# Optimization experiments

Measured on AMD Instinct MI355X. Metric: run time of the kernel, lower is better.

The kernel has to match this reference:

```python
import jax, jax.numpy as jnp
import numpy as np

H_SZ, W_SZ = 24, 24  # size for location=2 (H*W == N3)

def _ln(x, g, b, eps=1e-5):
    m = jnp.mean(x, axis=-1, keepdims=True)
    v = jnp.var(x, axis=-1, keepdims=True)
    return (x - m) / jnp.sqrt(v + eps) * g + b

def _cross_attn(value, x2, Wp, bp):
    # key = softmax(x2^T, dim=1) == softmax over channels; query = softmax over tokens
    k = jax.nn.softmax(x2, axis=2)   # [B,M,C], softmax over C
    q = jax.nn.softmax(x2, axis=1)   # [B,M,C], softmax over M
    ctx = jnp.einsum('bnc,bmc->bnm', value, k)   # value @ key
    att = jnp.einsum('bnm,bmc->bnc', ctx, q)     # context @ query
    return att @ Wp.T + bp

def _dwconv(x, Wdw, bdw, Hh, Ww):
    B, N, C = x.shape
    t = x.transpose(0, 2, 1).reshape(B, C, Hh, Ww)
    y = jax.lax.conv_general_dilated(t, Wdw, (1, 1), 'SAME',
                                     feature_group_count=C,
                                     dimension_numbers=('NCHW', 'OIHW', 'NCHW'))
    y = y + bdw[None, :, None, None]
    return y.reshape(B, C, N).transpose(0, 2, 1)

def setup_inputs() -> dict:
    key = jax.random.key(0)
    ks = jax.random.split(key, 16)
    B = 4; d0, d1, d2 = 128, 256, 512
    N1, N2, N3 = 96 * 96, 48 * 48, 24 * 24
    s = 0.02
    dh = 4 * d2
    inp = {}
    inp['x']  = jax.random.normal(ks[0], (B, N1, d0), jnp.float32)
    inp['x2'] = jax.random.normal(ks[1], (B, N2, d1), jnp.float32)
    inp['x3'] = jax.random.normal(ks[2], (B, N3, d2), jnp.float32)
    inp['W_lin']  = jax.random.normal(ks[3], (d2, d0)) * s   # linear: d0->d2
    inp['W_lin2'] = jax.random.normal(ks[4], (d2, d1)) * s   # linear2: d1->d2
    inp['W_lin3'] = jax.random.normal(ks[5], (d1, d0)) * s   # linear3: d0->d1
    inp['W_lin4'] = jax.random.normal(ks[6], (d2, d1)) * s   # linear4: d1->d2
    inp['w'] = jnp.ones((1,), jnp.float32)
    inp['Wp1'] = jax.random.normal(ks[7], (d2, d2)) * s;  inp['bp1'] = jnp.zeros((d2,))
    inp['Wp2'] = jax.random.normal(ks[8], (d2, d2)) * s;  inp['bp2'] = jnp.zeros((d2,))
    inp['Wp3'] = jax.random.normal(ks[9], (d1, d1)) * s;  inp['bp3'] = jnp.zeros((d1,))
    inp['Wp4'] = jax.random.normal(ks[10], (d2, d2)) * s; inp['bp4'] = jnp.zeros((d2,))
    inp['g_norm'] = jnp.ones((d2,)); inp['b_norm'] = jnp.zeros((d2,))
    inp['Wfc1'] = jax.random.normal(ks[11], (dh, d2)) * s; inp['bfc1'] = jnp.zeros((dh,))
    inp['Wdw']  = jax.random.normal(ks[12], (dh, 1, 3, 3)) * s; inp['bdw'] = jnp.zeros((dh,))
    inp['g_ln1'] = jnp.ones((dh,)); inp['b_ln1'] = jnp.zeros((dh,))
    inp['Wfc2'] = jax.random.normal(ks[13], (d2, dh)) * s; inp['bfc2'] = jnp.zeros((d2,))
    return inp

def reference(x, x2, x3, W_lin, W_lin2, W_lin3, W_lin4, w,
              Wp1, bp1, Wp2, bp2, Wp3, bp3, Wp4, bp4,
              g_norm, b_norm, Wfc1, bfc1, Wdw, bdw, g_ln1, b_ln1, Wfc2, bfc2):
    # location == 2 branch
    image  = x  @ W_lin.T    # [B,N1,d2]
    image2 = x2 @ W_lin2.T   # [B,N2,d2]
    image4 = x  @ W_lin3.T   # [B,N1,d1]
    atten1 = _cross_attn(x3, image,  Wp1, bp1)
    atten2 = _cross_attn(x3, image2, Wp2, bp2)
    a3 = _cross_attn(x2, image4, Wp3, bp3)   # [B,N2,d1]
    a3 = a3 @ W_lin4.T                        # [B,N2,d2]
    atten3 = _cross_attn(x3, a3, Wp4, bp4)    # [B,N3,d2]
    f = jax.nn.sigmoid(w)
    other = (1.0 - f) / 2.0
    atten_ = f * atten3 + other * atten2 + other * atten1
    atten = x3 + atten_
    an = _ln(atten, g_norm, b_norm)
    # MixFFN_skip (fc1 computed once; torch computes it twice with same result)
    h = an @ Wfc1.T + bfc1
    dw = _dwconv(h, Wdw, bdw, H_SZ, W_SZ)
    ax = jax.nn.gelu(_ln(dw + h, g_ln1, b_ln1), approximate=False)
    out = ax @ Wfc2.T + bfc2
    return atten + out
```

## Files before the change

### kernel.cpp

```cpp
#include <hip/hip_runtime.h>
#include <hip/hip_bf16.h>
#include <math.h>

typedef long long i64;
typedef __attribute__((ext_vector_type(8))) short short8v;
typedef __attribute__((ext_vector_type(4))) float float4v;

#define SPITCH 72
#define NCV 13

__device__ __forceinline__ float ldv(const void* p, i64 idx, int isBf16) {
  return isBf16 ? __bfloat162float(((const __hip_bfloat16*)p)[idx])
                : ((const float*)p)[idx];
}
__device__ __forceinline__ unsigned short bf16bits(float f) {
  __hip_bfloat16 h = __float2bfloat16(f);
  return *(unsigned short*)&h;
}
__device__ __forceinline__ float bits2f(unsigned short u) {
  union { unsigned int ui; float fl; } cv; cv.ui = ((unsigned int)u) << 16;
  return cv.fl;
}

__global__ void detect_dtype(const unsigned short* w, int* dt) {
  dt[0] = (w[0] == 0) ? 0 : 1;
}

struct CvArgs {
  const void* src[NCV];
  unsigned short* dst[NCV];
  i64 n[NCV];
  int blkStart[NCV + 1];
};
__global__ __launch_bounds__(256) void convert_many(const int* dt, CvArgs a) {
  int au = dt[0];
  int bid = blockIdx.x;
  int lo = 0;
  #pragma unroll
  for (int i = 0; i < NCV; ++i) if (bid >= a.blkStart[i + 1]) lo = i + 1;
  const void* s = a.src[lo];
  unsigned short* d = a.dst[lo];
  i64 n = a.n[lo];
  i64 base = ((i64)(bid - a.blkStart[lo]) * 256 + threadIdx.x) * 4;
  if (base + 4 <= n) {
    #pragma unroll
    for (int j = 0; j < 4; ++j) d[base + j] = bf16bits(ldv(s, base + j, au));
  } else {
    for (; base < n; ++base) d[base] = bf16bits(ldv(s, base, au));
  }
}

__global__ void transpose_dw(const int* dt, const void* Wdw, unsigned short* Wdwt) {
  int au = dt[0];
  int i = blockIdx.x * 256 + threadIdx.x;
  if (i >= 9 * 2048) return;
  int k = i / 2048, ch = i % 2048;
  Wdwt[i] = bf16bits(ldv(Wdw, (i64)ch * 9 + k, au));
}

__global__ __launch_bounds__(256) void gemm_mfma_bt(
    const int* dt,
    const unsigned short* A, i64 bsA,
    const unsigned short* Bt, i64 bsB,
    const void* bias, int biasDt,
    const void* add, int addDt, i64 bsAdd,
    void* C, i64 bsC, int outMode,
    int M, int N, int K, int flags,
    const void* wPtr, int alphaMode,
    float* csP, float* rsP)
{
  __shared__ unsigned short Ash[64 * SPITCH];
  __shared__ unsigned short Bsh[64 * SPITCH];
  __shared__ unsigned short LT[64 * SPITCH];

  const int au = dt[0];
  const int bDt = (biasDt == 2) ? au : biasDt;
  const int aDt = (addDt == 2) ? au : addDt;

  const int b  = blockIdx.z;
  const int m0 = blockIdx.y * 64;
  const int n0 = blockIdx.x * 64;
  const int t = threadIdx.x;
  const int lane = t & 63, wave = t >> 6;
  const int wr = (wave >> 1) * 32, wc = (wave & 1) * 32;
  const int quad = lane >> 4, l15 = lane & 15;
  const unsigned short* Ab = A + (i64)b * bsA;
  const unsigned short* Bb = Bt + (i64)b * bsB;
  const int sr = t >> 3, sg = (t & 7) * 8;

  float alpha = 1.0f;
  if (alphaMode) {
    float w0 = ldv(wPtr, 0, au);
    float f = 1.0f / (1.0f + expf(-w0));
    alpha = (alphaMode == 2) ? f : (1.0f - f) * 0.5f;
  }

  float4v acc00 = {0.f,0.f,0.f,0.f}, acc01 = {0.f,0.f,0.f,0.f};
  float4v acc10 = {0.f,0.f,0.f,0.f}, acc11 = {0.f,0.f,0.f,0.f};

  for (int k0 = 0; k0 < K; k0 += 64) {
    #pragma unroll
    for (int p = 0; p < 2; ++p) {
      int rr = sr + p * 32;
      *(short8v*)&Ash[rr * SPITCH + sg] = *(const short8v*)&Ab[(i64)(m0 + rr) * K + k0 + sg];
      *(short8v*)&Bsh[rr * SPITCH + sg] = *(const short8v*)&Bb[(i64)(n0 + rr) * K + k0 + sg];
    }
    __syncthreads();
    #pragma unroll
    for (int ks = 0; ks < 2; ++ks) {
      int ko = ks * 32 + quad * 8;
      short8v a0 = *(const short8v*)&Ash[(wr + l15) * SPITCH + ko];
      short8v a1 = *(const short8v*)&Ash[(wr + 16 + l15) * SPITCH + ko];
      short8v b0 = *(const short8v*)&Bsh[(wc + l15) * SPITCH + ko];
      short8v b1 = *(const short8v*)&Bsh[(wc + 16 + l15) * SPITCH + ko];
      acc00 = __builtin_amdgcn_mfma_f32_16x16x32_bf16(a0, b0, acc00, 0, 0, 0);
      acc01 = __builtin_amdgcn_mfma_f32_16x16x32_bf16(a0, b1, acc01, 0, 0, 0);
      acc10 = __builtin_amdgcn_mfma_f32_16x16x32_bf16(a1, b0, acc10, 0, 0, 0);
      acc11 = __builtin_amdgcn_mfma_f32_16x16x32_bf16(a1, b1, acc11, 0, 0, 0);
    }
    __syncthreads();
  }

  float* Cf = (float*)C;
  unsigned short* Ch = (unsigned short*)C;

  if (outMode == 2) {
    #pragma unroll
    for (int rg = 0; rg < 4; ++rg) {
      #pragma unroll
      for (int sub = 0; sub < 4; ++sub) {
        int lr = wr + quad * 4 + rg + (sub >> 1) * 16;
        int lc = wc + l15 + (sub & 1) * 16;
        float v = (sub == 0 ? acc00[rg] : sub == 1 ? acc01[rg] :
                   sub == 2 ? acc10[rg] : acc11[rg]) * alpha;
        if (bias) v += ldv(bias, n0 + lc, bDt);
        if (flags & 1) v = expf(v);
        LT[lc * SPITCH + lr] = bf16bits(v);
      }
    }
    __syncthreads();
    #pragma unroll
    for (int p = 0; p < 2; ++p) {
      int rr = sr + p * 32;
      short8v vv = *(short8v*)&LT[rr * SPITCH + sg];
      *(short8v*)(Ch + (i64)b * bsC + (i64)(n0 + rr) * M + m0 + sg) = vv;
    }
    if (csP) {
      if (t < 64) {
        const unsigned short* Lr = &LT[t * SPITCH];
        float s = 0.f;
        #pragma unroll
        for (int i = 0; i < 64; ++i) s += bits2f(Lr[i]);
        atomicAdd(&csP[(i64)b * N + n0 + t], s);
      } else if (t < 128) {
        int tok = t - 64;
        float s = 0.f;
        #pragma unroll
        for (int i = 0; i < 64; ++i) s += bits2f(LT[i * SPITCH + tok]);
        atomicAdd(&rsP[(i64)b * M + m0 + tok], s);
      }
    }
    return;
  }

  #pragma unroll
  for (int rg = 0; rg < 4; ++rg) {
    #pragma unroll
    for (int sub = 0; sub < 4; ++sub) {
      int lr = wr + quad * 4 + rg + (sub >> 1) * 16;
      int lc = wc + l15 + (sub & 1) * 16;
      int gi = m0 + lr, gj = n0 + lc;
      float v = (sub == 0 ? acc00[rg] : sub == 1 ? acc01[rg] :
                 sub == 2 ? acc10[rg] : acc11[rg]) * alpha;
      if (bias) v += ldv(bias, gj, bDt);
      if (add)  v += ldv(add, (i64)b * bsAdd + (i64)gi * N + gj, aDt);
      i64 idx = (i64)b * bsC + (i64)gi * N + gj;
      if (flags & 2) v += Cf[idx];
      if (flags & 1) v = expf(v);
      if (outMode == 1) Ch[idx] = bf16bits(v);
      else              Cf[idx] = v;
    }
  }
}

__global__ __launch_bounds__(256, 2) void softprod128_db(
    const unsigned short* Gt, const float* rs, float* Sraw,
    int C, i64 M, int splits, int mChunk)
{
  __shared__ unsigned short Ash[2][128 * SPITCH];
  __shared__ unsigned short Bsh[2][128 * SPITCH];
  const int b  = blockIdx.z / splits;
  const int sp = blockIdx.z % splits;
  const int nStrips = C >> 7;
  int rem = blockIdx.x, s0 = 0;
  while (rem >= nStrips - s0) { rem -= nStrips - s0; ++s0; }
  const int s1 = s0 + rem;
  const int c0 = s0 * 128;
  const int c1 = s1 * 128;

  const int t = threadIdx.x;
  const int lane = t & 63, wave = t >> 6;
  const int wrow = (wave >> 1) * 64, wcol = (wave & 1) * 64;
  const int quad = lane >> 4, l15 = lane & 15;
  const unsigned short* Gb = Gt + (i64)b * C * M;
  const float* rib = rs + (i64)b * M;
  const int sg = (t & 7) * 8;
  const int r4 = t >> 3;

  float4v acc[4][4];
  #pragma unroll
  for (int i = 0; i < 4; ++i)
    #pragma unroll
    for (int j = 0; j < 4; ++j)
      acc[i][j] = (float4v){0.f, 0.f, 0.f, 0.f};

  const i64 mBeg = (i64)sp * mChunk;
  const int nt = mChunk >> 6;

  const unsigned short* Arow = &Gb[(i64)(c0 + r4) * M + sg];
  const unsigned short* Brow = &Gb[(i64)(c1 + r4) * M + sg];

  short8v pa[4], pb[4];
  float rv[8];
  {
    i64 m0 = mBeg;
    #pragma unroll
    for (int p = 0; p < 4; ++p) {
      pa[p] = *(const short8v*)&Arow[(i64)32 * p * M + m0];
      pb[p] = *(const short8v*)&Brow[(i64)32 * p * M + m0];
    }
    #pragma unroll
    for (int j = 0; j < 8; ++j) {
      float rr_ = rsqrtf(rib[m0 + sg + j]);
      rv[j] = rr_ * rr_;
    }
  }

  int cur = 0;
  for (int tt = 0; tt < nt; ++tt) {
    #pragma unroll
    for (int p = 0; p < 4; ++p) {
      *(short8v*)&Ash[cur][(r4 + 32 * p) * SPITCH + sg] = pa[p];
      short8v sb;
      #pragma unroll
      for (int j = 0; j < 8; ++j)
        sb[j] = (short)bf16bits(bits2f((unsigned short)pb[p][j]) * rv[j]);
      *(short8v*)&Bsh[cur][(r4 + 32 * p) * SPITCH + sg] = sb;
    }
    __syncthreads();
    if (tt + 1 < nt) {
      i64 m0 = mBeg + (i64)(tt + 1) * 64;
      #pragma unroll
      for (int p = 0; p < 4; ++p) {
        pa[p] = *(const short8v*)&Arow[(i64)32 * p * M + m0];
        pb[p] = *(const short8v*)&Brow[(i64)32 * p * M + m0];
      }
      #pragma unroll
      for (int j = 0; j < 8; ++j) {
        float rr_ = rsqrtf(rib[m0 + sg + j]);
        rv[j] = rr_ * rr_;
      }
    }
    #pragma unroll
    for (int ks = 0; ks < 2; ++ks) {
      int ko = ks * 32 + quad * 8;
      short8v af[4], bfr[4];
      #pragma unroll
      for (int i = 0; i < 4; ++i) {
        af[i]  = *(const short8v*)&Ash[cur][(wrow + i * 16 + l15) * SPITCH + ko];
        bfr[i] = *(const short8v*)&Bsh[cur][(wcol + i * 16 + l15) * SPITCH + ko];
      }
      #pragma unroll
      for (int i = 0; i < 4; ++i)
        #pragma unroll
        for (int j = 0; j < 4; ++j)
          acc[i][j] = __builtin_amdgcn_mfma_f32_16x16x32_bf16(af[i], bfr[j], acc[i][j], 0, 0, 0);
    }
    cur ^= 1;
  }

  float* Sb = Sraw + (i64)b * C * C;
  #pragma unroll
  for (int i = 0; i < 4; ++i)
    #pragma unroll
    for (int rg = 0; rg < 4; ++rg) {
      int r = c0 + wrow + i * 16 + quad * 4 + rg;
      #pragma unroll
      for (int j = 0; j < 4; ++j) {
        int cc = c1 + wcol + j * 16 + l15;
        atomicAdd(&Sb[(i64)r * C + cc], acc[i][j][rg]);
      }
    }
}

__global__ void scale_S_sym_bf16(const float* Sraw, const float* cs,
                                 unsigned short* Sb, int C, i64 total) {
  i64 i = (i64)blockIdx.x * blockDim.x + threadIdx.x;
  if (i >= total) return;
  i64 cc2 = (i64)C * C;
  i64 b = i / cc2;
  i64 r = (i % cc2) / C;
  int cp = (int)(i % C);
  const float* Sb_ = Sraw + b * cc2;
  float v = (((int)r >> 6) <= (cp >> 6)) ? Sb_[r * C + cp] : Sb_[(i64)cp * C + r];
  Sb[i] = bf16bits(v / cs[b * C + cp]);
}

__global__ __launch_bounds__(256) void transpose_to_bf16(
    const float* T, unsigned short* Tt, int Nn) {
  __shared__ float tile[64][65];
  int b = blockIdx.z;
  int i0 = blockIdx.y * 64, j0 = blockIdx.x * 64;
  const float* Tb = T + (i64)b * Nn * Nn;
  unsigned short* Ttb = Tt + (i64)b * Nn * Nn;
  int t = threadIdx.x;
  int li = t >> 6, lj = t & 63;
  #pragma unroll
  for (int p = 0; p < 16; ++p)
    tile[li + p * 4][lj] = Tb[(i64)(i0 + li + p * 4) * Nn + j0 + lj];
  __syncthreads();
  #pragma unroll
  for (int p = 0; p < 16; ++p) {
    int row = li + p * 4;
    Ttb[(i64)(j0 + row) * Nn + i0 + lj] = bf16bits(tile[lj][row]);
  }
}

__global__ void combine_bias(const int* dt, const void* w, const void* bp1,
                             const void* bp2, const void* bp4, float* biasc) {
  int au = dt[0];
  int j = threadIdx.x;
  float w0 = ldv(w, 0, au);
  float f = 1.0f / (1.0f + expf(-w0));
  float other = (1.0f - f) * 0.5f;
  biasc[j] = f * ldv(bp4, j, au) + other * (ldv(bp1, j, au) + ldv(bp2, j, au));
}

__global__ __launch_bounds__(256) void layernorm512(const int* dt, const float* X,
                                                    const void* g, const void* be,
                                                    __hip_bfloat16* Y) {
  int au = dt[0];
  i64 row = blockIdx.x;
  const float* xr = X + row * 512;
  int t = threadIdx.x;
  float x0 = xr[t], x1 = xr[t + 256];
  float s = x0 + x1, q = x0 * x0 + x1 * x1;
  #pragma unroll
  for (int off = 32; off; off >>= 1) { s += __shfl_down(s, off); q += __shfl_down(q, off); }
  __shared__ float ws_[4], wq_[4];
  int lane = t & 63, wv = t >> 6;
  if (!lane) { ws_[wv] = s; wq_[wv] = q; }
  __syncthreads();
  float S = ws_[0] + ws_[1] + ws_[2] + ws_[3];
  float Q = wq_[0] + wq_[1] + wq_[2] + wq_[3];
  float mean = S * (1.f / 512.f);
  float var = Q * (1.f / 512.f) - mean * mean;
  float inv = rsqrtf(var + 1e-5f);
  Y[row * 512 + t]       = __float2bfloat16((x0 - mean) * inv * ldv(g, t, au) + ldv(be, t, au));
  Y[row * 512 + t + 256] = __float2bfloat16((x1 - mean) * inv * ldv(g, t + 256, au) + ldv(be, t + 256, au));
}

__global__ __launch_bounds__(256) void dwconv_ln_gelu(
    const int* dt,
    const unsigned short* h, const unsigned short* Wdwt, const void* bdw,
    const void* g, const void* be, unsigned short* ax)
{
  int au = dt[0];
  int n = blockIdx.x;
  int b = blockIdx.y;
  int y = n / 24, x = n % 24;
  const unsigned short* hb = h + (i64)b * 576 * 2048;
  int t = threadIdx.x;
  int ch0 = t * 8;

  float accv[8];
  #pragma unroll
  for (int j = 0; j < 8; ++j) accv[j] = ldv(bdw, ch0 + j, au);

  #pragma unroll
  for (int dy = 0; dy < 3; ++dy) {
    int yy = y + dy - 1;
    if (yy < 0 || yy >= 24) continue;
    #pragma unroll
    for (int dx = 0; dx < 3; ++dx) {
      int xx = x + dx - 1;
      if (xx < 0 || xx >= 24) continue;
      short8v hv = *(const short8v*)&hb[(i64)(yy * 24 + xx) * 2048 + ch0];
      short8v wv = *(const short8v*)&Wdwt[(i64)(dy * 3 + dx) * 2048 + ch0];
      #pragma unroll
      for (int j = 0; j < 8; ++j)
        accv[j] += bits2f((unsigned short)hv[j]) * bits2f((unsigned short)wv[j]);
    }
  }

  short8v hc = *(const short8v*)&hb[(i64)n * 2048 + ch0];
  float z[8];
  float s = 0.f, q = 0.f;
  #pragma unroll
  for (int j = 0; j < 8; ++j) {
    float zz = accv[j] + bits2f((unsigned short)hc[j]);
    z[j] = zz; s += zz; q += zz * zz;
  }

  #pragma unroll
  for (int off = 32; off; off >>= 1) { s += __shfl_down(s, off); q += __shfl_down(q, off); }
  __shared__ float ws_[4], wq_[4];
  int lane = t & 63, wv2 = t >> 6;
  if (!lane) { ws_[wv2] = s; wq_[wv2] = q; }
  __syncthreads();
  float S = ws_[0] + ws_[1] + ws_[2] + ws_[3];
  float Q = wq_[0] + wq_[1] + wq_[2] + wq_[3];
  float mean = S * (1.f / 2048.f);
  float var = Q * (1.f / 2048.f) - mean * mean;
  float inv = rsqrtf(var + 1e-5f);

  short8v ov;
  #pragma unroll
  for (int j = 0; j < 8; ++j) {
    float v = (z[j] - mean) * inv * ldv(g, ch0 + j, au) + ldv(be, ch0 + j, au);
    float gl = 0.5f * v * (1.0f + erff(v * 0.70710678118654752f));
    ov[j] = (short)bf16bits(gl);
  }
  *(short8v*)&ax[((i64)b * 576 + n) * 2048 + ch0] = ov;
}

extern "C" void kernel_launch(void* const* d_in, const int* in_sizes, int n_in,
                              void* d_out, int out_size, void* d_ws, size_t ws_size,
                              hipStream_t stream) {
  const int B = 4, N1 = 9216, N2 = 2304, N3 = 576;
  const int d0 = 128, d1 = 256, d2 = 512, dh = 2048;

  const void* x     = d_in[0];
  const void* x2    = d_in[1];
  const void* x3    = d_in[2];
  const void* Wlin  = d_in[3];
  const void* Wlin2 = d_in[4];
  const void* Wlin3 = d_in[5];
  const void* Wlin4 = d_in[6];
  const void* w     = d_in[7];
  const void* Wp1 = d_in[8];  const void* bp1 = d_in[9];
  const void* Wp2 = d_in[10]; const void* bp2 = d_in[11];
  const void* Wp3 = d_in[12]; const void* bp3 = d_in[13];
  const void* Wp4 = d_in[14]; const void* bp4 = d_in[15];
  const void* gnorm = d_in[16]; const void* bnorm = d_in[17];
  const void* Wfc1 = d_in[18]; const void* bfc1 = d_in[19];
  const void* Wdw  = d_in[20]; const void* bdw  = d_in[21];
  const void* gln1 = d_in[22]; const void* bln1 = d_in[23];
  const void* Wfc2 = d_in[24]; const void* bfc2 = d_in[25];

  char* base = (char*)d_ws;
  size_t o = 0;
  auto alloc = [&](size_t n) -> char* {
    char* r = base + o; o += (n + 255) & ~(size_t)255; return r;
  };

  int* dtFlag = (int*)alloc(256);
  char* arena = alloc((size_t)B * N1 * d2 * 2);
  float* rsBig   = (float*)alloc((size_t)B * N1 * 4);
  float* rsSmall = (float*)alloc((size_t)B * N2 * 4);
  size_t csBytes = (size_t)B * (d2 + d2 + d1 + d2) * 4;
  float* csAll = (float*)alloc(csBytes);
  float* cs1  = csAll;
  float* cs2  = cs1 + B * d2;
  float* cs4  = cs2 + B * d2;
  float* cs3b = cs4 + B * d1;
  float* Sraw  = (float*)alloc((size_t)B * d2 * d2 * 4);
  float* S3raw = (float*)alloc((size_t)B * d1 * d1 * 4);
  unsigned short* Sb16  = (unsigned short*)alloc((size_t)B * d2 * d2 * 2);
  unsigned short* S3b16 = (unsigned short*)alloc((size_t)B * d1 * d1 * 2);
  unsigned short* U3t   = (unsigned short*)alloc((size_t)B * d1 * d1 * 2);
  float* T     = (float*)alloc((size_t)B * d2 * d2 * 4);
  float* biasc = (float*)alloc((size_t)d2 * 4);
  unsigned short* xb  = (unsigned short*)alloc((size_t)B * N1 * d0 * 2);
  unsigned short* x2b = (unsigned short*)alloc((size_t)B * N2 * d1 * 2);
  unsigned short* x3b = (unsigned short*)alloc((size_t)B * N3 * d2 * 2);
  unsigned short* Wlinb  = (unsigned short*)alloc((size_t)d2 * d0 * 2);
  unsigned short* Wlin2b = (unsigned short*)alloc((size_t)d2 * d1 * 2);
  unsigned short* Wlin3b = (unsigned short*)alloc((size_t)d1 * d0 * 2);
  unsigned short* Wlin4b = (unsigned short*)alloc((size_t)d2 * d1 * 2);
  unsigned short* Wp1b = (unsigned short*)alloc((size_t)d2 * d2 * 2);
  unsigned short* Wp2b = (unsigned short*)alloc((size_t)d2 * d2 * 2);
  unsigned short* Wp3b = (unsigned short*)alloc((size_t)d1 * d1 * 2);
  unsigned short* Wp4b = (unsigned short*)alloc((size_t)d2 * d2 * 2);
  unsigned short* Wfc1b = (unsigned short*)alloc((size_t)dh * d2 * 2);
  unsigned short* Wfc2b = (unsigned short*)alloc((size_t)d2 * dh * 2);
  unsigned short* Wdwt  = (unsigned short*)alloc((size_t)9 * dh * 2);

  unsigned short* Et1    = (unsigned short*)arena;
  unsigned short* Et4    = (unsigned short*)arena;
  unsigned short* a3buf  = (unsigned short*)(arena + 18874368);
  unsigned short* EtA3b  = (unsigned short*)arena;
  unsigned short* Et2    = (unsigned short*)arena;
  float*          atten  = (float*)arena;
  __hip_bfloat16* an     = (__hip_bfloat16*)(arena + 4718592);
  unsigned short* hbuf   = (unsigned short*)(arena + 7077888);
  unsigned short* axb    = (unsigned short*)(arena + 16515072);
  unsigned short* Tt     = (unsigned short*)(arena + 28573696);

  detect_dtype<<<dim3(1), dim3(1), 0, stream>>>((const unsigned short*)w, dtFlag);
  hipMemsetAsync(csAll, 0, csBytes, stream);

  {
    CvArgs a;
    const void* srcs[NCV] = { x, x2, x3, Wlin, Wlin2, Wlin3, Wlin4,
                              Wp1, Wp2, Wp3, Wp4, Wfc1, Wfc2 };
    unsigned short* dsts[NCV] = { xb, x2b, x3b, Wlinb, Wlin2b, Wlin3b, Wlin4b,
                                  Wp1b, Wp2b, Wp3b, Wp4b, Wfc1b, Wfc2b };
    i64 ns[NCV] = { (i64)B*N1*d0, (i64)B*N2*d1, (i64)B*N3*d2,
                    (i64)d2*d0, (i64)d2*d1, (i64)d1*d0, (i64)d2*d1,
                    (i64)d2*d2, (i64)d2*d2, (i64)d1*d1, (i64)d2*d2,
                    (i64)dh*d2, (i64)d2*dh };
    int cum = 0;
    for (int i = 0; i < NCV; ++i) {
      a.src[i] = srcs[i]; a.dst[i] = dsts[i]; a.n[i] = ns[i];
      a.blkStart[i] = cum;
      cum += (int)((ns[i] + 1023) / 1024);
    }
    a.blkStart[NCV] = cum;
    convert_many<<<dim3(cum), dim3(256), 0, stream>>>(dtFlag, a);
    transpose_dw<<<dim3((9 * dh + 255) / 256), dim3(256), 0, stream>>>(dtFlag, Wdw, Wdwt);
  }

  auto gemm64 = [&](const unsigned short* A_, i64 bsA,
                    const unsigned short* Bt_, i64 bsB,
                    const void* bias_, int biasDt,
                    const void* add_, int addDt, i64 bsAdd,
                    void* C_, i64 bsC, int outMode,
                    int M_, int N_, int K_, int flags, int alphaMode,
                    float* csP = nullptr, float* rsP = nullptr) {
    gemm_mfma_bt<<<dim3(N_ / 64, M_ / 64, B), dim3(256), 0, stream>>>(
        dtFlag, A_, bsA, Bt_, bsB, bias_, biasDt, add_, addDt, bsAdd,
        C_, bsC, outMode, M_, N_, K_, flags, w, alphaMode, csP, rsP);
  };

  auto softtail = [&](unsigned short* Et, float* cs, float* rsArr,
                      float* SrawB, unsigned short* SbB, int C, int M, int splits) {
    hipMemsetAsync(SrawB, 0, (size_t)B * C * C * 4, stream);
    int nStrips = C / 128;
    int nPairs = nStrips * (nStrips + 1) / 2;
    softprod128_db<<<dim3(nPairs, 1, B * splits), dim3(256), 0, stream>>>(
        Et, rsArr, SrawB, C, M, splits, M / splits);
    i64 totS = (i64)B * C * C;
    scale_S_sym_bf16<<<dim3((unsigned)((totS + 255) / 256)), dim3(256), 0, stream>>>(
        SrawB, cs, SbB, C, totS);
  };

  hipMemsetAsync(rsBig, 0, (size_t)B * N1 * 4, stream);
  gemm64(xb, (i64)N1 * d0, Wlinb, 0, nullptr, 0, nullptr, 0, 0,
         Et1, (i64)N1 * d2, 2, N1, d2, d0, 1, 0, cs1, rsBig);
  softtail(Et1, cs1, rsBig, Sraw, Sb16, d2, N1, 12);
  gemm64(Sb16, (i64)d2 * d2, Wp1b, 0, nullptr, 0, nullptr, 0, 0,
         T, (i64)d2 * d2, 0, d2, d2, d2, 0, 1);

  hipMemsetAsync(rsBig, 0, (size_t)B * N1 * 4, stream);
  gemm64(xb, (i64)N1 * d0, Wlin3b, 0, nullptr, 0, nullptr, 0, 0,
         Et4, (i64)N1 * d1, 2, N1, d1, d0, 1, 0, cs4, rsBig);
  softtail(Et4, cs4, rsBig, S3raw, S3b16, d1, N1, 36);
  gemm64(S3b16, (i64)d1 * d1, Wp3b, 0, nullptr, 0, nullptr, 0, 0,
         U3t, (i64)d1 * d1, 2, d1, d1, d1, 0, 0);
  gemm64(x2b, (i64)N2 * d1, U3t, (i64)d1 * d1, bp3, 2, nullptr, 0, 0,
         a3buf, (i64)N2 * d1, 1, N2, d1, d1, 0, 0);
  hipMemsetAsync(rsSmall, 0, (size_t)B * N2 * 4, stream);
  gemm64(a3buf, (i64)N2 * d1, Wlin4b, 0, nullptr, 0, nullptr, 0, 0,
         EtA3b, (i64)N2 * d2, 2, N2, d2, d1, 1, 0, cs3b, rsSmall);
  softtail(EtA3b, cs3b, rsSmall, Sraw, Sb16, d2, N2, 12);
  gemm64(Sb16, (i64)d2 * d2, Wp4b, 0, nullptr, 0, nullptr, 0, 0,
         T, (i64)d2 * d2, 0, d2, d2, d2, 2, 2);

  hipMemsetAsync(rsSmall, 0, (size_t)B * N2 * 4, stream);
  gemm64(x2b, (i64)N2 * d1, Wlin2b, 0, nullptr, 0, nullptr, 0, 0,
         Et2, (i64)N2 * d2, 2, N2, d2, d1, 1, 0, cs2, rsSmall);
  softtail(Et2, cs2, rsSmall, Sraw, Sb16, d2, N2, 12);
  gemm64(Sb16, (i64)d2 * d2, Wp2b, 0, nullptr, 0, nullptr, 0, 0,
         T, (i64)d2 * d2, 0, d2, d2, d2, 2, 1);

  transpose_to_bf16<<<dim3(d2 / 64, d2 / 64, B), dim3(256), 0, stream>>>(T, Tt, d2);
  combine_bias<<<dim3(1), dim3(d2), 0, stream>>>(dtFlag, w, bp1, bp2, bp4, biasc);

  gemm64(x3b, (i64)N3 * d2, Tt, (i64)d2 * d2, biasc, 0, x3, 2, (i64)N3 * d2,
         atten, (i64)N3 * d2, 0, N3, d2, d2, 0, 0);

  layernorm512<<<dim3(B * N3), dim3(256), 0, stream>>>(dtFlag, atten, gnorm, bnorm, an);

  gemm64((const unsigned short*)an, (i64)N3 * d2, Wfc1b, 0, bfc1, 2, nullptr, 0, 0,
         hbuf, (i64)N3 * dh, 1, N3, dh, d2, 0, 0);

  dwconv_ln_gelu<<<dim3(N3, B), dim3(256), 0, stream>>>(
      dtFlag, hbuf, Wdwt, bdw, gln1, bln1, axb);

  gemm64(axb, (i64)N3 * dh, Wfc2b, 0, bfc2, 2,
         atten, 0, (i64)N3 * d2,
         d_out, (i64)N3 * d2, 0, N3, d2, dh, 0, 0);

  (void)in_sizes; (void)n_in; (void)out_size; (void)ws_size;
}
```

Before: 562.1 us.

## Remap softprod blocks per XCD and prefetch two tiles ahead

```diff
diff --git a/kernel.cpp b/kernel.cpp
--- a/kernel.cpp
+++ b/kernel.cpp
@@ -185,14 +185,22 @@
 
 __global__ __launch_bounds__(256, 2) void softprod128_db(
     const unsigned short* Gt, const float* rs, float* Sraw,
-    int C, i64 M, int splits, int mChunk)
+    int C, i64 M, int splits, int mChunk, int nPairs)
 {
   __shared__ unsigned short Ash[2][128 * SPITCH];
   __shared__ unsigned short Bsh[2][128 * SPITCH];
-  const int b  = blockIdx.z / splits;
-  const int sp = blockIdx.z % splits;
+
+  const int bid = blockIdx.x;
+  const int xcd = bid & 7;
+  const int q = bid >> 3;
+  const int gHi = q / nPairs;
+  const int pr = q - gHi * nPairs;
+  const int g = gHi * 8 + xcd;
+  const int b  = g / splits;
+  const int sp = g - b * splits;
+
   const int nStrips = C >> 7;
-  int rem = blockIdx.x, s0 = 0;
+  int rem = pr, s0 = 0;
   while (rem >= nStrips - s0) { rem -= nStrips - s0; ++s0; }
   const int s1 = s0 + rem;
   const int c0 = s0 * 128;
@@ -220,55 +228,41 @@
   const unsigned short* Arow = &Gb[(i64)(c0 + r4) * M + sg];
   const unsigned short* Brow = &Gb[(i64)(c1 + r4) * M + sg];
 
-  short8v pa[4], pb[4];
-  float rv[8];
-  {
-    i64 m0 = mBeg;
-    #pragma unroll
-    for (int p = 0; p < 4; ++p) {
-      pa[p] = *(const short8v*)&Arow[(i64)32 * p * M + m0];
-      pb[p] = *(const short8v*)&Brow[(i64)32 * p * M + m0];
+  short8v pa0[4], pb0[4], pa1[4], pb1[4];
+  float rv0[8], rv1[8];
+
+  auto loadF = [&](i64 m0, short8v* pa, short8v* pb, float* rv) {
+    #pragma unroll
+    for (int pp = 0; pp < 4; ++pp) {
+      pa[pp] = *(const short8v*)&Arow[(i64)32 * pp * M + m0];
+      pb[pp] = *(const short8v*)&Brow[(i64)32 * pp * M + m0];
     }
     #pragma unroll
     for (int j = 0; j < 8; ++j) {
-      float rr_ = rsqrtf(rib[m0 + sg + j]);
-      rv[j] = rr_ * rr_;
-    }
-  }
-
-  int cur = 0;
-  for (int tt = 0; tt < nt; ++tt) {
-    #pragma unroll
-    for (int p = 0; p < 4; ++p) {
-      *(short8v*)&Ash[cur][(r4 + 32 * p) * SPITCH + sg] = pa[p];
+      float r_ = rsqrtf(rib[m0 + sg + j]);
+      rv[j] = r_ * r_;
+    }
+  };
+  auto stageF = [&](int bi, const short8v* pa, const short8v* pb, const float* rv) {
+    #pragma unroll
+    for (int pp = 0; pp < 4; ++pp) {
+      *(short8v*)&Ash[bi][(r4 + 32 * pp) * SPITCH + sg] = pa[pp];
       short8v sb;
       #pragma unroll
       for (int j = 0; j < 8; ++j)
-        sb[j] = (short)bf16bits(bits2f((unsigned short)pb[p][j]) * rv[j]);
-      *(short8v*)&Bsh[cur][(r4 + 32 * p) * SPITCH + sg] = sb;
-    }
-    __syncthreads();
-    if (tt + 1 < nt) {
-      i64 m0 = mBeg + (i64)(tt + 1) * 64;
-      #pragma unroll
-      for (int p = 0; p < 4; ++p) {
-        pa[p] = *(const short8v*)&Arow[(i64)32 * p * M + m0];
-        pb[p] = *(const short8v*)&Brow[(i64)32 * p * M + m0];
-      }
-      #pragma unroll
-      for (int j = 0; j < 8; ++j) {
-        float rr_ = rsqrtf(rib[m0 + sg + j]);
-        rv[j] = rr_ * rr_;
-      }
-    }
+        sb[j] = (short)bf16bits(bits2f((unsigned short)pb[pp][j]) * rv[j]);
+      *(short8v*)&Bsh[bi][(r4 + 32 * pp) * SPITCH + sg] = sb;
+    }
+  };
+  auto mfmaF = [&](int bi) {
     #pragma unroll
     for (int ks = 0; ks < 2; ++ks) {
       int ko = ks * 32 + quad * 8;
       short8v af[4], bfr[4];
       #pragma unroll
       for (int i = 0; i < 4; ++i) {
-        af[i]  = *(const short8v*)&Ash[cur][(wrow + i * 16 + l15) * SPITCH + ko];
-        bfr[i] = *(const short8v*)&Bsh[cur][(wcol + i * 16 + l15) * SPITCH + ko];
+        af[i]  = *(const short8v*)&Ash[bi][(wrow + i * 16 + l15) * SPITCH + ko];
+        bfr[i] = *(const short8v*)&Bsh[bi][(wcol + i * 16 + l15) * SPITCH + ko];
       }
       #pragma unroll
       for (int i = 0; i < 4; ++i)
@@ -276,7 +270,23 @@
         for (int j = 0; j < 4; ++j)
           acc[i][j] = __builtin_amdgcn_mfma_f32_16x16x32_bf16(af[i], bfr[j], acc[i][j], 0, 0, 0);
     }
-    cur ^= 1;
+  };
+
+  loadF(mBeg, pa0, pb0, rv0);
+  if (nt > 1) loadF(mBeg + 64, pa1, pb1, rv1);
+
+  for (int tt = 0; tt < nt; tt += 2) {
+    stageF(0, pa0, pb0, rv0);
+    asm volatile("s_waitcnt lgkmcnt(0)" ::: "memory");
+    __builtin_amdgcn_s_barrier();
+    if (tt + 2 < nt) loadF(mBeg + (i64)(tt + 2) * 64, pa0, pb0, rv0);
+    mfmaF(0);
+    if (tt + 1 >= nt) break;
+    stageF(1, pa1, pb1, rv1);
+    asm volatile("s_waitcnt lgkmcnt(0)" ::: "memory");
+    __builtin_amdgcn_s_barrier();
+    if (tt + 3 < nt) loadF(mBeg + (i64)(tt + 3) * 64, pa1, pb1, rv1);
+    mfmaF(1);
   }
 
   float* Sb = Sraw + (i64)b * C * C;
@@ -538,8 +548,9 @@
     hipMemsetAsync(SrawB, 0, (size_t)B * C * C * 4, stream);
     int nStrips = C / 128;
     int nPairs = nStrips * (nStrips + 1) / 2;
-    softprod128_db<<<dim3(nPairs, 1, B * splits), dim3(256), 0, stream>>>(
-        Et, rsArr, SrawB, C, M, splits, M / splits);
+    int nBlk = nPairs * B * splits;
+    softprod128_db<<<dim3(nBlk), dim3(256), 0, stream>>>(
+        Et, rsArr, SrawB, C, M, splits, M / splits, nPairs);
     i64 totS = (i64)B * C * C;
     scale_S_sym_bf16<<<dim3((unsigned)((totS + 255) / 256)), dim3(256), 0, stream>>>(
         SrawB, cs, SbB, C, totS);
```

Result: slower. 588.6 us (+4.7%).
